# Optimization experiments

Hardware: AMD Instinct MI355X
Metric: run time of the kernel (lower is better)

## Reference

```python
import jax, jax.numpy as jnp
import numpy as np

N_NODES = 8192
IN_DIM = 20000
HID = 256
LAT = 64
N_EDGES = 262144


def setup_inputs() -> dict:
    key = jax.random.key(0)
    ks = jax.random.split(key, 12)
    s_in = 1.0 / np.sqrt(IN_DIM)
    s_h = 1.0 / np.sqrt(HID)
    s_l = 1.0 / np.sqrt(LAT)
    return {
        "x": jax.random.normal(ks[0], (N_NODES, IN_DIM), jnp.float32),
        "edge_index": jax.random.randint(ks[1], (2, N_EDGES), 0, N_NODES, jnp.int64 if jax.config.jax_enable_x64 else jnp.int32),
        "w_gcn": jax.random.uniform(ks[2], (IN_DIM, HID), jnp.float32, -s_in, s_in),
        "b_gcn": jnp.zeros((HID,), jnp.float32),
        "w_enc": jax.random.uniform(ks[3], (HID, LAT), jnp.float32, -s_h, s_h),
        "b_enc": jax.random.uniform(ks[4], (LAT,), jnp.float32, -s_h, s_h),
        "w_d1": jax.random.uniform(ks[5], (LAT, HID), jnp.float32, -s_l, s_l),
        "b_d1": jax.random.uniform(ks[6], (HID,), jnp.float32, -s_l, s_l),
        "w_d2": jax.random.uniform(ks[7], (HID, IN_DIM), jnp.float32, -s_h, s_h),
        "b_d2": jax.random.uniform(ks[8], (IN_DIM,), jnp.float32, -s_h, s_h),
    }


def _gcn_conv(x, edge_index, w, b):
    """PyG GCNConv (add_self_loops=True, normalize=True): A_hat @ (x W) + b."""
    n = x.shape[0]
    h = x @ w  # [N, HID] -- project first (in_dim >> out_dim)
    loops = jnp.arange(n, dtype=edge_index.dtype)
    row = jnp.concatenate([edge_index[0], loops])  # source nodes
    col = jnp.concatenate([edge_index[1], loops])  # target nodes
    deg = jax.ops.segment_sum(jnp.ones_like(col, dtype=h.dtype), col, num_segments=n)
    dinv = jnp.where(deg > 0, jax.lax.rsqrt(deg), 0.0)
    norm = dinv[row] * dinv[col]  # [E+N]
    msg = h[row] * norm[:, None]  # gather + scale
    out = jax.ops.segment_sum(msg, col, num_segments=n)  # scatter-add
    return out + b


def reference(x, edge_index, w_gcn, b_gcn, w_enc, b_enc, w_d1, b_d1, w_d2, b_d2):
    # Encoder: GCNConv -> ReLU -> (Dropout: eval no-op) -> Linear
    h = _gcn_conv(x, edge_index, w_gcn, b_gcn)
    latent = jax.nn.relu(h) @ w_enc + b_enc  # [N, LAT]
    # Decoder: Linear -> ReLU -> (Dropout) -> Linear
    recon = jax.nn.relu(latent @ w_d1 + b_d1) @ w_d2 + b_d2  # [N, IN_DIM]
    return recon, latent
```

## Files before the change

### kernel.cpp

```cpp
#include <hip/hip_runtime.h>
#include <stdint.h>

typedef short short8 __attribute__((ext_vector_type(8)));
typedef float f32x4 __attribute__((ext_vector_type(4)));

#define N_NODES 8192
#define IN_DIM 20000
#define HIDDEN 256
#define LATENT 64
#define N_EDGES 262144
#define K_STEPS 625
#define SPLIT0_STEPS 312
#define RECON_ELEMS (8192LL * 20000LL)
#define WD2T_ROWS 20096
#define NSUB3 313

static __device__ __forceinline__ unsigned short f2bf(float f) {
  union { float f; unsigned int u; } v;
  v.f = f;
  unsigned int u = v.u;
  return (unsigned short)((u + 0x7FFFu + ((u >> 16) & 1u)) >> 16);
}

__global__ void k_count(const int* __restrict__ col, int* __restrict__ cnt) {
  int e = blockIdx.x * 256 + threadIdx.x;
  if (e < N_EDGES) atomicAdd(&cnt[col[e]], 1);
}

__global__ void k_dinv(const int* __restrict__ cnt, float* __restrict__ dinv) {
  int i = blockIdx.x * 256 + threadIdx.x;
  if (i < N_NODES) dinv[i] = rsqrtf((float)(cnt[i] + 1));
}

__global__ void k_scan(const int* __restrict__ cnt, int* __restrict__ offs,
                       int* __restrict__ cursor) {
  __shared__ int ps[256];
  int t = threadIdx.x;
  int local[32];
  int s = 0;
#pragma unroll
  for (int i = 0; i < 32; ++i) { local[i] = cnt[t * 32 + i]; s += local[i]; }
  ps[t] = s;
  __syncthreads();
  for (int d = 1; d < 256; d <<= 1) {
    int v = (t >= d) ? ps[t - d] : 0;
    __syncthreads();
    ps[t] += v;
    __syncthreads();
  }
  int pre = (t == 0) ? 0 : ps[t - 1];
#pragma unroll
  for (int i = 0; i < 32; ++i) {
    offs[t * 32 + i] = pre;
    cursor[t * 32 + i] = pre;
    pre += local[i];
  }
  if (t == 255) offs[N_NODES] = pre;
}

__global__ void k_fill(const int* __restrict__ row, const int* __restrict__ col,
                       int* __restrict__ cursor, int* __restrict__ csr_src) {
  int e = blockIdx.x * 256 + threadIdx.x;
  if (e < N_EDGES) {
    int c = col[e];
    int pos = atomicAdd(&cursor[c], 1);
    csr_src[pos] = row[e];
  }
}

__global__ void k_pack_wgcn(const float* __restrict__ w, unsigned short* __restrict__ pk) {
  int s = blockIdx.x;
  int t = threadIdx.x;
  int k0 = s * 32;
  unsigned int packed[16];
#pragma unroll
  for (int j = 0; j < 16; ++j) {
    float a = w[(size_t)(k0 + 2 * j) * HIDDEN + t];
    float b = w[(size_t)(k0 + 2 * j + 1) * HIDDEN + t];
    packed[j] = (unsigned)f2bf(a) | ((unsigned)f2bf(b) << 16);
  }
  uint4* dst = (uint4*)(pk + ((size_t)s * HIDDEN + t) * 32);
#pragma unroll
  for (int j = 0; j < 4; ++j)
    dst[j] = make_uint4(packed[4 * j], packed[4 * j + 1], packed[4 * j + 2], packed[4 * j + 3]);
}

__global__ void k_twd2(const float* __restrict__ wd2, unsigned short* __restrict__ wd2t) {
  __shared__ float tile[HIDDEN * 64];
  int n0 = blockIdx.x * 64;
  int t = threadIdx.x;
  int tk = t >> 6;
  int tn = t & 63;
#pragma unroll 4
  for (int kb = 0; kb < 64; ++kb) {
    int k = kb * 4 + tk;
    int n = n0 + tn;
    tile[k * 64 + tn] = (n < IN_DIM) ? wd2[(size_t)k * IN_DIM + n] : 0.0f;
  }
  __syncthreads();
  int rl = t >> 2;
  int q = t & 3;
  unsigned int packed[32];
#pragma unroll
  for (int j = 0; j < 32; ++j) {
    float a = tile[(q * 64 + 2 * j) * 64 + rl];
    float b = tile[(q * 64 + 2 * j + 1) * 64 + rl];
    packed[j] = (unsigned)f2bf(a) | ((unsigned)f2bf(b) << 16);
  }
  int rs = rl & 7;
  uint4* dst = (uint4*)(wd2t + (size_t)(n0 + rl) * HIDDEN + q * 64);
#pragma unroll
  for (int j = 0; j < 8; ++j)
    dst[j ^ rs] = make_uint4(packed[4 * j], packed[4 * j + 1], packed[4 * j + 2], packed[4 * j + 3]);
}

__global__ __launch_bounds__(256, 2)
void k_gemm1(const float* __restrict__ x, const unsigned short* __restrict__ wpk,
             float* __restrict__ h0p) {
  const int m0 = blockIdx.x * 32;
  const int split = blockIdx.y;
  const int s_beg = split ? SPLIT0_STEPS : 0;
  const int s_end = split ? K_STEPS : SPLIT0_STEPS;

  const int t = threadIdx.x;
  const int lane = t & 63;
  const int w = t >> 6;
  const int lr = lane & 15;
  const int lg = lane >> 4;

  __shared__ unsigned short Alds[2][32 * 40];
  __shared__ unsigned short Blds[2][256 * 32];

  const int arow = t >> 3;
  const int ak = (t & 7) * 4;
  const float* xrow = x + (size_t)(m0 + arow) * IN_DIM + ak;
  const int bsw = ((t ^ (t >> 2)) & 3);

  f32x4 acc[2][4];
#pragma unroll
  for (int i = 0; i < 2; ++i)
#pragma unroll
    for (int j = 0; j < 4; ++j) acc[i][j] = (f32x4){0.f, 0.f, 0.f, 0.f};

  float4 areg;
  uint4 breg0, breg1, breg2, breg3;

  areg = *(const float4*)(xrow + (size_t)s_beg * 32);
  {
    const uint4* bp = (const uint4*)(wpk + ((size_t)s_beg * 256 + t) * 32);
    breg0 = bp[0]; breg1 = bp[1]; breg2 = bp[2]; breg3 = bp[3];
  }
  {
    uint2 ap;
    ap.x = (unsigned)f2bf(areg.x) | ((unsigned)f2bf(areg.y) << 16);
    ap.y = (unsigned)f2bf(areg.z) | ((unsigned)f2bf(areg.w) << 16);
    *(uint2*)&Alds[0][arow * 40 + ak] = ap;
    uint4* br = (uint4*)&Blds[0][t * 32];
    br[0 ^ bsw] = breg0; br[1 ^ bsw] = breg1; br[2 ^ bsw] = breg2; br[3 ^ bsw] = breg3;
  }
  __syncthreads();

  int cur = 0;
  for (int s = s_beg; s < s_end; ++s) {
    bool more = (s + 1 < s_end);
    if (more) {
      areg = *(const float4*)(xrow + (size_t)(s + 1) * 32);
      const uint4* bp = (const uint4*)(wpk + ((size_t)(s + 1) * 256 + t) * 32);
      breg0 = bp[0]; breg1 = bp[1]; breg2 = bp[2]; breg3 = bp[3];
    }
    {
      short8 a0 = *(const short8*)&Alds[cur][lr * 40 + lg * 8];
      short8 a1 = *(const short8*)&Alds[cur][(16 + lr) * 40 + lg * 8];
#pragma unroll
      for (int ct = 0; ct < 4; ++ct) {
        int n = w * 64 + ct * 16 + lr;
        int sw = ((n ^ (n >> 2)) & 3);
        short8 b = *(const short8*)&Blds[cur][n * 32 + ((lg ^ sw) * 8)];
        acc[0][ct] = __builtin_amdgcn_mfma_f32_16x16x32_bf16(a0, b, acc[0][ct], 0, 0, 0);
        acc[1][ct] = __builtin_amdgcn_mfma_f32_16x16x32_bf16(a1, b, acc[1][ct], 0, 0, 0);
      }
    }
    if (more) {
      __syncthreads();
      int nb = cur ^ 1;
      uint2 ap;
      ap.x = (unsigned)f2bf(areg.x) | ((unsigned)f2bf(areg.y) << 16);
      ap.y = (unsigned)f2bf(areg.z) | ((unsigned)f2bf(areg.w) << 16);
      *(uint2*)&Alds[nb][arow * 40 + ak] = ap;
      uint4* br = (uint4*)&Blds[nb][t * 32];
      br[0 ^ bsw] = breg0; br[1 ^ bsw] = breg1; br[2 ^ bsw] = breg2; br[3 ^ bsw] = breg3;
      __syncthreads();
      cur = nb;
    }
  }

  float* outp = h0p + (size_t)split * (N_NODES * HIDDEN) + (size_t)m0 * HIDDEN;
#pragma unroll
  for (int mt = 0; mt < 2; ++mt)
#pragma unroll
    for (int ct = 0; ct < 4; ++ct) {
      int col = w * 64 + ct * 16 + lr;
#pragma unroll
      for (int r = 0; r < 4; ++r) {
        int rowi = mt * 16 + lg * 4 + r;
        outp[rowi * HIDDEN + col] = acc[mt][ct][r];
      }
    }
}

__global__ void k_sum(const float* __restrict__ p, float* __restrict__ h0) {
  int i = blockIdx.x * 256 + threadIdx.x;
  float4 a = ((const float4*)p)[i];
  float4 b = ((const float4*)p)[i + (N_NODES * HIDDEN / 4)];
  float4 r;
  r.x = a.x + b.x; r.y = a.y + b.y; r.z = a.z + b.z; r.w = a.w + b.w;
  ((float4*)h0)[i] = r;
}

__global__ void k_agg(const float* __restrict__ h0, const float* __restrict__ dinv,
                      const int* __restrict__ offs, const int* __restrict__ csr_src,
                      const float* __restrict__ bias, float* __restrict__ hrelu) {
  int c = blockIdx.x;
  int t = threadIdx.x;
  float dc = dinv[c];
  float acc = h0[(size_t)c * HIDDEN + t] * dc * dc;
  int beg = offs[c], end = offs[c + 1];
  for (int i = beg; i < end; ++i) {
    int r = csr_src[i];
    float wgt = dinv[r] * dc;
    acc += h0[(size_t)r * HIDDEN + t] * wgt;
  }
  float v = acc + bias[t];
  hrelu[(size_t)c * HIDDEN + t] = v > 0.f ? v : 0.f;
}

__global__ void k_enc(const float* __restrict__ hrelu, const float* __restrict__ w_enc,
                      const float* __restrict__ b_enc, float* __restrict__ latent) {
  __shared__ float hrow[4 * HIDDEN];
  int nb = blockIdx.x * 4;
  int t = threadIdx.x;
#pragma unroll
  for (int j = 0; j < 4; ++j) hrow[j * HIDDEN + t] = hrelu[(size_t)(nb + j) * HIDDEN + t];
  __syncthreads();
  int lat = t & 63;
  int nl = t >> 6;
  float acc = b_enc[lat];
#pragma unroll 8
  for (int k = 0; k < HIDDEN; ++k)
    acc += hrow[nl * HIDDEN + k] * w_enc[k * LATENT + lat];
  latent[(size_t)(nb + nl) * LATENT + lat] = acc;
}

__global__ void k_dec1(const float* __restrict__ latent, const float* __restrict__ w_d1,
                       const float* __restrict__ b_d1, unsigned short* __restrict__ hid2) {
  __shared__ float lrow[4 * LATENT];
  int nb = blockIdx.x * 4;
  int t = threadIdx.x;
  lrow[t] = latent[(size_t)nb * LATENT + t];
  __syncthreads();
  float b = b_d1[t];
  float a0 = b, a1 = b, a2 = b, a3 = b;
#pragma unroll 8
  for (int k = 0; k < LATENT; ++k) {
    float wv = w_d1[k * HIDDEN + t];
    a0 += lrow[k] * wv;
    a1 += lrow[LATENT + k] * wv;
    a2 += lrow[2 * LATENT + k] * wv;
    a3 += lrow[3 * LATENT + k] * wv;
  }
  hid2[(size_t)nb * HIDDEN + t]       = f2bf(a0 > 0.f ? a0 : 0.f);
  hid2[(size_t)(nb + 1) * HIDDEN + t] = f2bf(a1 > 0.f ? a1 : 0.f);
  hid2[(size_t)(nb + 2) * HIDDEN + t] = f2bf(a2 > 0.f ? a2 : 0.f);
  hid2[(size_t)(nb + 3) * HIDDEN + t] = f2bf(a3 > 0.f ? a3 : 0.f);
}

__global__ __launch_bounds__(512, 4)
void k_gemm3(const unsigned short* __restrict__ hid2, const unsigned short* __restrict__ wd2t,
             const float* __restrict__ b_d2, float* __restrict__ recon) {
  __shared__ unsigned short Bl[2][64 * 256];
  __shared__ float TB[8 * 512];
  const int t = threadIdx.x;
  const int lane = t & 63;
  const int wid = t >> 6;
  const int wm = wid >> 1;
  const int wn = wid & 1;
  const int lr = lane & 15;
  const int lg = lane >> 4;
  const int m0 = blockIdx.x * 128;
  const int chunk = blockIdx.y;
  const int s0 = (NSUB3 * chunk) >> 3;
  const int s1 = (NSUB3 * (chunk + 1)) >> 3;

  short8 a[2][8];
#pragma unroll
  for (int mt = 0; mt < 2; ++mt)
#pragma unroll
    for (int ks = 0; ks < 8; ++ks)
      a[mt][ks] = *(const short8*)(hid2 + (size_t)(m0 + wm * 32 + mt * 16 + lr) * 256 + ks * 32 + lg * 8);

  auto stage = [&](int sub, int buf) {
#pragma unroll
    for (int i = 0; i < 4; ++i) {
      const unsigned short* g = wd2t + (size_t)sub * (64 * 256) + ((wid * 4 + i) * 512 + lane * 8);
      unsigned short* l = &Bl[buf][(wid * 4 + i) * 512];
      __builtin_amdgcn_global_load_lds(
          (const __attribute__((address_space(1))) unsigned int*)g,
          (__attribute__((address_space(3))) unsigned int*)l, 16, 0, 0);
    }
  };

  stage(s0, 0);
  __syncthreads();

  int cur = 0;
  for (int sub = s0; sub < s1; ++sub) {
    if (sub + 1 < s1) stage(sub + 1, cur ^ 1);

    f32x4 acc[2][2];
#pragma unroll
    for (int i = 0; i < 2; ++i)
#pragma unroll
      for (int j = 0; j < 2; ++j) acc[i][j] = (f32x4){0.f, 0.f, 0.f, 0.f};

    const int rl0 = wn * 32 + lr;
    const int rl1 = rl0 + 16;
#pragma unroll
    for (int ks = 0; ks < 8; ++ks) {
      short8 b0 = *(const short8*)&Bl[cur][rl0 * 256 + (((ks * 4 + lg) ^ (lr & 7)) << 3)];
      short8 b1 = *(const short8*)&Bl[cur][rl1 * 256 + (((ks * 4 + lg) ^ (lr & 7)) << 3)];
      acc[0][0] = __builtin_amdgcn_mfma_f32_16x16x32_bf16(a[0][ks], b0, acc[0][0], 0, 0, 0);
      acc[1][0] = __builtin_amdgcn_mfma_f32_16x16x32_bf16(a[1][ks], b0, acc[1][0], 0, 0, 0);
      acc[0][1] = __builtin_amdgcn_mfma_f32_16x16x32_bf16(a[0][ks], b1, acc[0][1], 0, 0, 0);
      acc[1][1] = __builtin_amdgcn_mfma_f32_16x16x32_bf16(a[1][ks], b1, acc[1][1], 0, 0, 0);
    }

    const int cg = (lane & 7) * 4;
    const int gc = sub * 64 + wn * 32 + cg;
    f32x4 bias4 = (f32x4){0.f, 0.f, 0.f, 0.f};
    if (gc < IN_DIM) bias4 = *(const f32x4*)&b_d2[gc];
    float* TBw = TB + wid * 512;
#pragma unroll
    for (int mt = 0; mt < 2; ++mt) {
#pragma unroll
      for (int nt = 0; nt < 2; ++nt)
#pragma unroll
        for (int r = 0; r < 4; ++r) {
          int row = lg * 4 + r;
          TBw[row * 32 + ((nt * 16 + lr) ^ (((row >> 2) & 1) << 4))] = acc[mt][nt][r];
        }
#pragma unroll
      for (int p = 0; p < 2; ++p) {
        int row = p * 8 + (lane >> 3);
        f32x4 v = *(const f32x4*)&TBw[row * 32 + (cg ^ (((row >> 2) & 1) << 4))];
        if (gc < IN_DIM) {
          int gr = m0 + wm * 32 + mt * 16 + row;
          *(f32x4*)&recon[(size_t)gr * IN_DIM + gc] = v + bias4;
        }
      }
    }
    __syncthreads();
    cur ^= 1;
  }
}

extern "C" void kernel_launch(void* const* d_in, const int* in_sizes, int n_in,
                              void* d_out, int out_size, void* d_ws, size_t ws_size,
                              hipStream_t stream) {
  const float* x     = (const float*)d_in[0];
  const int*   edge  = (const int*)d_in[1];
  const float* w_gcn = (const float*)d_in[2];
  const float* b_gcn = (const float*)d_in[3];
  const float* w_enc = (const float*)d_in[4];
  const float* b_enc = (const float*)d_in[5];
  const float* w_d1  = (const float*)d_in[6];
  const float* b_d1  = (const float*)d_in[7];
  const float* w_d2  = (const float*)d_in[8];
  const float* b_d2  = (const float*)d_in[9];
  float* out = (float*)d_out;
  (void)in_sizes; (void)n_in; (void)out_size; (void)ws_size;

  char* ws = (char*)d_ws;
  size_t o = 0;
  auto alloc = [&](size_t bytes) {
    char* p = ws + o;
    o += (bytes + 255) & ~(size_t)255;
    return p;
  };
  unsigned short* wpk  = (unsigned short*)alloc((size_t)K_STEPS * HIDDEN * 32 * 2);
  unsigned short* wd2t = (unsigned short*)alloc((size_t)WD2T_ROWS * HIDDEN * 2);
  float* h0p  = (float*)alloc((size_t)2 * N_NODES * HIDDEN * 4);
  float* h0   = (float*)alloc((size_t)N_NODES * HIDDEN * 4);
  float* hrel = (float*)alloc((size_t)N_NODES * HIDDEN * 4);
  unsigned short* hid2 = (unsigned short*)alloc((size_t)N_NODES * HIDDEN * 2);
  int* cnt    = (int*)alloc(N_NODES * 4);
  float* dinv = (float*)alloc(N_NODES * 4);
  int* offs   = (int*)alloc((N_NODES + 1) * 4);
  int* cursor = (int*)alloc(N_NODES * 4);
  int* csr    = (int*)alloc((size_t)N_EDGES * 4);

  const int* erow = edge;
  const int* ecol = edge + N_EDGES;

  hipMemsetAsync(cnt, 0, N_NODES * 4, stream);
  k_count<<<N_EDGES / 256, 256, 0, stream>>>(ecol, cnt);
  k_scan<<<1, 256, 0, stream>>>(cnt, offs, cursor);
  k_dinv<<<N_NODES / 256, 256, 0, stream>>>(cnt, dinv);
  k_fill<<<N_EDGES / 256, 256, 0, stream>>>(erow, ecol, cursor, csr);
  k_pack_wgcn<<<K_STEPS, 256, 0, stream>>>(w_gcn, wpk);
  k_twd2<<<WD2T_ROWS / 64, 256, 0, stream>>>(w_d2, wd2t);
  k_gemm1<<<dim3(N_NODES / 32, 2), 256, 0, stream>>>(x, wpk, h0p);
  k_sum<<<(N_NODES * HIDDEN / 4) / 256, 256, 0, stream>>>(h0p, h0);
  k_agg<<<N_NODES, 256, 0, stream>>>(h0, dinv, offs, csr, b_gcn, hrel);
  float* latent = out + RECON_ELEMS;
  k_enc<<<N_NODES / 4, 256, 0, stream>>>(hrel, w_enc, b_enc, latent);
  k_dec1<<<N_NODES / 4, 256, 0, stream>>>(latent, w_d1, b_d1, hid2);
  k_gemm3<<<dim3(N_NODES / 128, 8), 512, 0, stream>>>(hid2, wd2t, b_d2, out);
}
```

Before: 721.1 us.

## Retile both GEMMs, use direct global-to-LDS loads for W_gcn, 4-way split-K

```diff
diff --git a/kernel.cpp b/kernel.cpp
--- a/kernel.cpp
+++ b/kernel.cpp
@@ -10,7 +10,6 @@
 #define LATENT 64
 #define N_EDGES 262144
 #define K_STEPS 625
-#define SPLIT0_STEPS 312
 #define RECON_ELEMS (8192LL * 20000LL)
 #define WD2T_ROWS 20096
 #define NSUB3 313
@@ -79,10 +78,11 @@
     float b = w[(size_t)(k0 + 2 * j + 1) * HIDDEN + t];
     packed[j] = (unsigned)f2bf(a) | ((unsigned)f2bf(b) << 16);
   }
+  int sw = (t >> 1) & 3;
   uint4* dst = (uint4*)(pk + ((size_t)s * HIDDEN + t) * 32);
 #pragma unroll
   for (int j = 0; j < 4; ++j)
-    dst[j] = make_uint4(packed[4 * j], packed[4 * j + 1], packed[4 * j + 2], packed[4 * j + 3]);
+    dst[j ^ sw] = make_uint4(packed[4 * j], packed[4 * j + 1], packed[4 * j + 2], packed[4 * j + 3]);
 }
 
 __global__ void k_twd2(const float* __restrict__ wd2, unsigned short* __restrict__ wd2t) {
@@ -114,27 +114,28 @@
     dst[j ^ rs] = make_uint4(packed[4 * j], packed[4 * j + 1], packed[4 * j + 2], packed[4 * j + 3]);
 }
 
-__global__ __launch_bounds__(256, 2)
+__global__ __launch_bounds__(512, 4)
 void k_gemm1(const float* __restrict__ x, const unsigned short* __restrict__ wpk,
              float* __restrict__ h0p) {
-  const int m0 = blockIdx.x * 32;
+  const int m0 = blockIdx.x * 64;
   const int split = blockIdx.y;
-  const int s_beg = split ? SPLIT0_STEPS : 0;
-  const int s_end = split ? K_STEPS : SPLIT0_STEPS;
+  const int s_beg = (K_STEPS * split) >> 2;
+  const int s_end = (K_STEPS * (split + 1)) >> 2;
 
   const int t = threadIdx.x;
   const int lane = t & 63;
-  const int w = t >> 6;
+  const int wid = t >> 6;
+  const int wm = wid >> 2;
+  const int wn = wid & 3;
   const int lr = lane & 15;
   const int lg = lane >> 4;
 
-  __shared__ unsigned short Alds[2][32 * 40];
+  __shared__ unsigned short Alds[2][64 * 40];
   __shared__ unsigned short Blds[2][256 * 32];
 
   const int arow = t >> 3;
   const int ak = (t & 7) * 4;
   const float* xrow = x + (size_t)(m0 + arow) * IN_DIM + ak;
-  const int bsw = ((t ^ (t >> 2)) & 3);
 
   f32x4 acc[2][4];
 #pragma unroll
@@ -142,68 +143,65 @@
 #pragma unroll
     for (int j = 0; j < 4; ++j) acc[i][j] = (f32x4){0.f, 0.f, 0.f, 0.f};
 
-  float4 areg;
-  uint4 breg0, breg1, breg2, breg3;
-
-  areg = *(const float4*)(xrow + (size_t)s_beg * 32);
-  {
-    const uint4* bp = (const uint4*)(wpk + ((size_t)s_beg * 256 + t) * 32);
-    breg0 = bp[0]; breg1 = bp[1]; breg2 = bp[2]; breg3 = bp[3];
-  }
+  auto stageB = [&](int s, int buf) {
+    const unsigned short* g = wpk + (size_t)s * (HIDDEN * 32) + wid * 512 + lane * 8;
+    __builtin_amdgcn_global_load_lds(
+        (const __attribute__((address_space(1))) unsigned int*)g,
+        (__attribute__((address_space(3))) unsigned int*)&Blds[buf][wid * 512], 16, 0, 0);
+    __builtin_amdgcn_global_load_lds(
+        (const __attribute__((address_space(1))) unsigned int*)(g + 4096),
+        (__attribute__((address_space(3))) unsigned int*)&Blds[buf][4096 + wid * 512], 16, 0, 0);
+  };
+
+  float4 areg = *(const float4*)(xrow + (size_t)s_beg * 32);
+  stageB(s_beg, 0);
   {
     uint2 ap;
     ap.x = (unsigned)f2bf(areg.x) | ((unsigned)f2bf(areg.y) << 16);
     ap.y = (unsigned)f2bf(areg.z) | ((unsigned)f2bf(areg.w) << 16);
     *(uint2*)&Alds[0][arow * 40 + ak] = ap;
-    uint4* br = (uint4*)&Blds[0][t * 32];
-    br[0 ^ bsw] = breg0; br[1 ^ bsw] = breg1; br[2 ^ bsw] = breg2; br[3 ^ bsw] = breg3;
   }
   __syncthreads();
 
   int cur = 0;
   for (int s = s_beg; s < s_end; ++s) {
-    bool more = (s + 1 < s_end);
+    const bool more = (s + 1 < s_end);
     if (more) {
       areg = *(const float4*)(xrow + (size_t)(s + 1) * 32);
-      const uint4* bp = (const uint4*)(wpk + ((size_t)(s + 1) * 256 + t) * 32);
-      breg0 = bp[0]; breg1 = bp[1]; breg2 = bp[2]; breg3 = bp[3];
+      stageB(s + 1, cur ^ 1);
     }
     {
-      short8 a0 = *(const short8*)&Alds[cur][lr * 40 + lg * 8];
-      short8 a1 = *(const short8*)&Alds[cur][(16 + lr) * 40 + lg * 8];
-#pragma unroll
-      for (int ct = 0; ct < 4; ++ct) {
-        int n = w * 64 + ct * 16 + lr;
-        int sw = ((n ^ (n >> 2)) & 3);
-        short8 b = *(const short8*)&Blds[cur][n * 32 + ((lg ^ sw) * 8)];
-        acc[0][ct] = __builtin_amdgcn_mfma_f32_16x16x32_bf16(a0, b, acc[0][ct], 0, 0, 0);
-        acc[1][ct] = __builtin_amdgcn_mfma_f32_16x16x32_bf16(a1, b, acc[1][ct], 0, 0, 0);
+      short8 a0 = *(const short8*)&Alds[cur][(wm * 32 + lr) * 40 + lg * 8];
+      short8 a1 = *(const short8*)&Alds[cur][(wm * 32 + 16 + lr) * 40 + lg * 8];
+#pragma unroll
+      for (int nt = 0; nt < 4; ++nt) {
+        int n = wn * 64 + nt * 16 + lr;
+        short8 b = *(const short8*)&Blds[cur][n * 32 + ((lg ^ ((n >> 1) & 3)) * 8)];
+        acc[0][nt] = __builtin_amdgcn_mfma_f32_16x16x32_bf16(a0, b, acc[0][nt], 0, 0, 0);
+        acc[1][nt] = __builtin_amdgcn_mfma_f32_16x16x32_bf16(a1, b, acc[1][nt], 0, 0, 0);
       }
     }
+    __syncthreads();
     if (more) {
-      __syncthreads();
-      int nb = cur ^ 1;
       uint2 ap;
       ap.x = (unsigned)f2bf(areg.x) | ((unsigned)f2bf(areg.y) << 16);
       ap.y = (unsigned)f2bf(areg.z) | ((unsigned)f2bf(areg.w) << 16);
-      *(uint2*)&Alds[nb][arow * 40 + ak] = ap;
-      uint4* br = (uint4*)&Blds[nb][t * 32];
-      br[0 ^ bsw] = breg0; br[1 ^ bsw] = breg1; br[2 ^ bsw] = breg2; br[3 ^ bsw] = breg3;
+      *(uint2*)&Alds[cur ^ 1][arow * 40 + ak] = ap;
       __syncthreads();
-      cur = nb;
-    }
+    }
+    cur ^= 1;
   }
 
   float* outp = h0p + (size_t)split * (N_NODES * HIDDEN) + (size_t)m0 * HIDDEN;
 #pragma unroll
   for (int mt = 0; mt < 2; ++mt)
 #pragma unroll
-    for (int ct = 0; ct < 4; ++ct) {
-      int col = w * 64 + ct * 16 + lr;
+    for (int nt = 0; nt < 4; ++nt) {
+      int col = wn * 64 + nt * 16 + lr;
 #pragma unroll
       for (int r = 0; r < 4; ++r) {
-        int rowi = mt * 16 + lg * 4 + r;
-        outp[rowi * HIDDEN + col] = acc[mt][ct][r];
+        int rowi = wm * 32 + mt * 16 + lg * 4 + r;
+        outp[rowi * HIDDEN + col] = acc[mt][nt][r];
       }
     }
 }
@@ -212,8 +210,13 @@
   int i = blockIdx.x * 256 + threadIdx.x;
   float4 a = ((const float4*)p)[i];
   float4 b = ((const float4*)p)[i + (N_NODES * HIDDEN / 4)];
+  float4 c = ((const float4*)p)[i + 2 * (N_NODES * HIDDEN / 4)];
+  float4 d = ((const float4*)p)[i + 3 * (N_NODES * HIDDEN / 4)];
   float4 r;
-  r.x = a.x + b.x; r.y = a.y + b.y; r.z = a.z + b.z; r.w = a.w + b.w;
+  r.x = (a.x + b.x) + (c.x + d.x);
+  r.y = (a.y + b.y) + (c.y + d.y);
+  r.z = (a.z + b.z) + (c.z + d.z);
+  r.w = (a.w + b.w) + (c.w + d.w);
   ((float4*)h0)[i] = r;
 }
 
@@ -274,11 +277,11 @@
   hid2[(size_t)(nb + 3) * HIDDEN + t] = f2bf(a3 > 0.f ? a3 : 0.f);
 }
 
-__global__ __launch_bounds__(512, 4)
+__global__ __launch_bounds__(256, 2)
 void k_gemm3(const unsigned short* __restrict__ hid2, const unsigned short* __restrict__ wd2t,
              const float* __restrict__ b_d2, float* __restrict__ recon) {
   __shared__ unsigned short Bl[2][64 * 256];
-  __shared__ float TB[8 * 512];
+  __shared__ float TB[4 * 512];
   const int t = threadIdx.x;
   const int lane = t & 63;
   const int wid = t >> 6;
@@ -291,18 +294,18 @@
   const int s0 = (NSUB3 * chunk) >> 3;
   const int s1 = (NSUB3 * (chunk + 1)) >> 3;
 
-  short8 a[2][8];
-#pragma unroll
-  for (int mt = 0; mt < 2; ++mt)
+  short8 a[4][8];
+#pragma unroll
+  for (int mt = 0; mt < 4; ++mt)
 #pragma unroll
     for (int ks = 0; ks < 8; ++ks)
-      a[mt][ks] = *(const short8*)(hid2 + (size_t)(m0 + wm * 32 + mt * 16 + lr) * 256 + ks * 32 + lg * 8);
+      a[mt][ks] = *(const short8*)(hid2 + (size_t)(m0 + wm * 64 + mt * 16 + lr) * 256 + ks * 32 + lg * 8);
 
   auto stage = [&](int sub, int buf) {
 #pragma unroll
-    for (int i = 0; i < 4; ++i) {
-      const unsigned short* g = wd2t + (size_t)sub * (64 * 256) + ((wid * 4 + i) * 512 + lane * 8);
-      unsigned short* l = &Bl[buf][(wid * 4 + i) * 512];
+    for (int i = 0; i < 8; ++i) {
+      const unsigned short* g = wd2t + (size_t)sub * (64 * 256) + ((wid * 8 + i) * 512 + lane * 8);
+      unsigned short* l = &Bl[buf][(wid * 8 + i) * 512];
       __builtin_amdgcn_global_load_lds(
           (const __attribute__((address_space(1))) unsigned int*)g,
           (__attribute__((address_space(3))) unsigned int*)l, 16, 0, 0);
@@ -316,22 +319,24 @@
   for (int sub = s0; sub < s1; ++sub) {
     if (sub + 1 < s1) stage(sub + 1, cur ^ 1);
 
-    f32x4 acc[2][2];
-#pragma unroll
-    for (int i = 0; i < 2; ++i)
-#pragma unroll
-      for (int j = 0; j < 2; ++j) acc[i][j] = (f32x4){0.f, 0.f, 0.f, 0.f};
+    f32x4 acc[4][2];
+#pragma unroll
+    for (int i = 0; i < 4; ++i) {
+      acc[i][0] = (f32x4){0.f, 0.f, 0.f, 0.f};
+      acc[i][1] = (f32x4){0.f, 0.f, 0.f, 0.f};
+    }
 
     const int rl0 = wn * 32 + lr;
     const int rl1 = rl0 + 16;
 #pragma unroll
     for (int ks = 0; ks < 8; ++ks) {
-      short8 b0 = *(const short8*)&Bl[cur][rl0 * 256 + (((ks * 4 + lg) ^ (lr & 7)) << 3)];
-      short8 b1 = *(const short8*)&Bl[cur][rl1 * 256 + (((ks * 4 + lg) ^ (lr & 7)) << 3)];
-      acc[0][0] = __builtin_amdgcn_mfma_f32_16x16x32_bf16(a[0][ks], b0, acc[0][0], 0, 0, 0);
-      acc[1][0] = __builtin_amdgcn_mfma_f32_16x16x32_bf16(a[1][ks], b0, acc[1][0], 0, 0, 0);
-      acc[0][1] = __builtin_amdgcn_mfma_f32_16x16x32_bf16(a[0][ks], b1, acc[0][1], 0, 0, 0);
-      acc[1][1] = __builtin_amdgcn_mfma_f32_16x16x32_bf16(a[1][ks], b1, acc[1][1], 0, 0, 0);
+      short8 b0 = *(const short8*)&Bl[cur][rl0 * 256 + (((ks * 4 + lg) ^ (rl0 & 7)) << 3)];
+      short8 b1 = *(const short8*)&Bl[cur][rl1 * 256 + (((ks * 4 + lg) ^ (rl1 & 7)) << 3)];
+#pragma unroll
+      for (int mt = 0; mt < 4; ++mt) {
+        acc[mt][0] = __builtin_amdgcn_mfma_f32_16x16x32_bf16(a[mt][ks], b0, acc[mt][0], 0, 0, 0);
+        acc[mt][1] = __builtin_amdgcn_mfma_f32_16x16x32_bf16(a[mt][ks], b1, acc[mt][1], 0, 0, 0);
+      }
     }
 
     const int cg = (lane & 7) * 4;
@@ -340,7 +345,7 @@
     if (gc < IN_DIM) bias4 = *(const f32x4*)&b_d2[gc];
     float* TBw = TB + wid * 512;
 #pragma unroll
-    for (int mt = 0; mt < 2; ++mt) {
+    for (int mt = 0; mt < 4; ++mt) {
 #pragma unroll
       for (int nt = 0; nt < 2; ++nt)
 #pragma unroll
@@ -353,7 +358,7 @@
         int row = p * 8 + (lane >> 3);
         f32x4 v = *(const f32x4*)&TBw[row * 32 + (cg ^ (((row >> 2) & 1) << 4))];
         if (gc < IN_DIM) {
-          int gr = m0 + wm * 32 + mt * 16 + row;
+          int gr = m0 + wm * 64 + mt * 16 + row;
           *(f32x4*)&recon[(size_t)gr * IN_DIM + gc] = v + bias4;
         }
       }
@@ -388,7 +393,7 @@
   };
   unsigned short* wpk  = (unsigned short*)alloc((size_t)K_STEPS * HIDDEN * 32 * 2);
   unsigned short* wd2t = (unsigned short*)alloc((size_t)WD2T_ROWS * HIDDEN * 2);
-  float* h0p  = (float*)alloc((size_t)2 * N_NODES * HIDDEN * 4);
+  float* h0p  = (float*)alloc((size_t)4 * N_NODES * HIDDEN * 4);
   float* h0   = (float*)alloc((size_t)N_NODES * HIDDEN * 4);
   float* hrel = (float*)alloc((size_t)N_NODES * HIDDEN * 4);
   unsigned short* hid2 = (unsigned short*)alloc((size_t)N_NODES * HIDDEN * 2);
@@ -408,11 +413,11 @@
   k_fill<<<N_EDGES / 256, 256, 0, stream>>>(erow, ecol, cursor, csr);
   k_pack_wgcn<<<K_STEPS, 256, 0, stream>>>(w_gcn, wpk);
   k_twd2<<<WD2T_ROWS / 64, 256, 0, stream>>>(w_d2, wd2t);
-  k_gemm1<<<dim3(N_NODES / 32, 2), 256, 0, stream>>>(x, wpk, h0p);
+  k_gemm1<<<dim3(N_NODES / 64, 4), 512, 0, stream>>>(x, wpk, h0p);
   k_sum<<<(N_NODES * HIDDEN / 4) / 256, 256, 0, stream>>>(h0p, h0);
   k_agg<<<N_NODES, 256, 0, stream>>>(h0, dinv, offs, csr, b_gcn, hrel);
   float* latent = out + RECON_ELEMS;
   k_enc<<<N_NODES / 4, 256, 0, stream>>>(hrel, w_enc, b_enc, latent);
   k_dec1<<<N_NODES / 4, 256, 0, stream>>>(latent, w_d1, b_d1, hid2);
-  k_gemm3<<<dim3(N_NODES / 128, 8), 512, 0, stream>>>(hid2, wd2t, b_d2, out);
-}
+  k_gemm3<<<dim3(N_NODES / 128, 8), 256, 0, stream>>>(hid2, wd2t, b_d2, out);
+}
```

Result: faster. 630.1 us (-12.6%).
